# Optimization experiments

Measured on AMD Instinct MI355X. Metric: run time of the kernel, lower is better.

The kernel has to match this reference:

```python
import jax, jax.numpy as jnp
import numpy as np
from math import sqrt

B, L, H, D = 4, 4096, 8, 64
FACTOR = 5


def setup_inputs():
    key = jax.random.key(0)
    k1, k2, k3, k4 = jax.random.split(key, 4)
    queries = jax.random.normal(k1, (B, L, H, D), dtype=jnp.float32)
    keys = jax.random.normal(k2, (B, L, H, D), dtype=jnp.float32)
    values = jax.random.normal(k3, (B, L, H, D), dtype=jnp.float32)
    sample_k = min(FACTOR * int(np.ceil(np.log(L))), L)  # U_part = 45
    index_sample = jax.random.randint(k4, (L, sample_k), 0, L)
    return {"queries": queries, "keys": keys, "values": values,
            "index_sample": index_sample}


def reference(queries, keys, values, index_sample):
    Bq, L_Q, Hq, Dq = queries.shape
    L_K = keys.shape[1]
    Q = jnp.transpose(queries, (0, 2, 1, 3))  # [B,H,L_Q,D]
    K = jnp.transpose(keys, (0, 2, 1, 3))     # [B,H,L_K,D]
    V = jnp.transpose(values, (0, 2, 1, 3))   # [B,H,L_K,D]
    n_top = min(FACTOR * int(np.ceil(np.log(L_Q))), L_Q)  # u = 45

    # --- _prob_QK: randomly-sampled QK scoring + top-k query selection ---
    K_sample = K[:, :, index_sample, :]                       # [B,H,L_Q,sample_k,D]
    Q_K_sample = jnp.einsum('bhld,bhlkd->bhlk', Q, K_sample)  # [B,H,L_Q,sample_k]
    M = Q_K_sample.max(-1) - Q_K_sample.sum(-1) / L_K         # sparsity measure
    _, M_top = jax.lax.top_k(M, n_top)                        # [B,H,u] query indices
    Q_reduce = jnp.take_along_axis(Q, M_top[..., None], axis=2)  # [B,H,u,D]
    scores = jnp.einsum('bhud,bhkd->bhuk', Q_reduce, K)       # [B,H,u,L_K]

    # scale = 1/sqrt(D) (self.scale is None)
    scores = scores * (1.0 / sqrt(Dq))

    # --- ProbMask (mask_flag=True): causal, key j masked if j > query idx ---
    mask = jnp.arange(L_K)[None, None, None, :] > M_top[..., None]
    scores = jnp.where(mask, -jnp.inf, scores)
    attn = jax.nn.softmax(scores, axis=-1)                    # [B,H,u,L_K]

    # --- initial context (masked case): cumulative sum of V over time ---
    context = jnp.cumsum(V, axis=2)                           # [B,H,L_Q,D]

    # --- scatter attn@V into the selected query positions ---
    upd = jnp.einsum('bhuk,bhkd->bhud', attn, V)              # [B,H,u,D]
    b_idx = jnp.arange(Bq)[:, None, None]
    h_idx = jnp.arange(Hq)[None, :, None]
    context = context.at[b_idx, h_idx, M_top].set(upd)
    return context  # [B,H,L_Q,D], as returned by the torch module
```

## Files before the change

### kernel.cpp

```cpp
#include <hip/hip_runtime.h>

#define NB 4
#define LSEQ 4096
#define NH 8
#define ND 64
#define NSAMP 45
#define NTOP 45

typedef float f32x4 __attribute__((ext_vector_type(4)));

__global__ __launch_bounds__(256) void prep_kernel(
        const int* __restrict__ idxS, int* __restrict__ sortedPack) {
    int t = threadIdx.x;
    int l = blockIdx.x * 256 + t;
    const int* is = idxS + (size_t)l * NSAMP;
    __shared__ int cnt[256][17];
    #pragma unroll
    for (int c = 0; c < 16; ++c) cnt[t][c] = 0;
    for (int s = 0; s < NSAMP; ++s) cnt[t][is[s] >> 8] += 1;
    int run = 0;
    #pragma unroll
    for (int c = 0; c < 16; ++c) { int v = cnt[t][c]; cnt[t][c] = run; run += v; }
    for (int s = 0; s < NSAMP; ++s) {
        int idx = is[s];
        int pos = cnt[t][idx >> 8]++;
        sortedPack[(size_t)l * NSAMP + pos] = (idx << 8) | s;
    }
}

__global__ __launch_bounds__(256, 1) void compute_M_kernel(
        const float* __restrict__ Q,
        const float* __restrict__ K,
        const int* __restrict__ sortedPack,
        float* __restrict__ Mout) {
    int xcd = blockIdx.x & 7;
    int sub = blockIdx.x >> 3;
    int bh  = (xcd << 2) | (sub & 3);
    int lt  = sub >> 2;
    int b = bh >> 3, h = bh & 7;
    int t = threadIdx.x;
    int l0 = (lt << 9) + t;
    int l1 = l0 + 256;

    __shared__ float Ks[256 * 68];
    __shared__ float Plds[512 * 45];

    f32x4 qa[16], qb[16];
    {
        const f32x4* qp0 = reinterpret_cast<const f32x4*>(
            Q + (((size_t)b * LSEQ + l0) * NH + h) * ND);
        const f32x4* qp1 = reinterpret_cast<const f32x4*>(
            Q + (((size_t)b * LSEQ + l1) * NH + h) * ND);
        #pragma unroll
        for (int i = 0; i < 16; ++i) qa[i] = __builtin_nontemporal_load(qp0 + i);
        #pragma unroll
        for (int i = 0; i < 16; ++i) qb[i] = __builtin_nontemporal_load(qp1 + i);
    }

    auto dotQK = [&](const f32x4 (&q4)[16], const float* kr) -> float {
        const f32x4* k4 = reinterpret_cast<const f32x4*>(kr);
        float w[32];
        #pragma unroll
        for (int i = 0; i < 8; ++i) {
            f32x4 a = q4[i], bb = k4[i], c = q4[i + 8], d4 = k4[i + 8];
            w[4 * i + 0] = __fadd_rn(__fmul_rn(a.x, bb.x), __fmul_rn(c.x, d4.x));
            w[4 * i + 1] = __fadd_rn(__fmul_rn(a.y, bb.y), __fmul_rn(c.y, d4.y));
            w[4 * i + 2] = __fadd_rn(__fmul_rn(a.z, bb.z), __fmul_rn(c.z, d4.z));
            w[4 * i + 3] = __fadd_rn(__fmul_rn(a.w, bb.w), __fmul_rn(c.w, d4.w));
        }
        #pragma unroll
        for (int off = 16; off; off >>= 1) {
            #pragma unroll
            for (int i = 0; i < off; ++i) w[i] = __fadd_rn(w[i], w[i + off]);
        }
        return w[0];
    };

    const int* sp0 = sortedPack + (size_t)l0 * NSAMP;
    const int* sp1 = sortedPack + (size_t)l1 * NSAMP;
    int ptr0 = 0, ptr1 = 0;
    int pk0 = sp0[0], pk1 = sp1[0];

    size_t kbh = ((size_t)b * LSEQ * NH + h) * ND;

    for (int c = 0; c < 16; ++c) {
        #pragma unroll
        for (int i = 0; i < 16; ++i) {
            int flat = i * 256 + t;
            int row = flat >> 4, col = flat & 15;
            f32x4 v = *reinterpret_cast<const f32x4*>(
                K + kbh + (size_t)(c * 256 + row) * (NH * ND) + col * 4);
            *reinterpret_cast<f32x4*>(&Ks[row * 68 + col * 4]) = v;
        }
        __syncthreads();

        while ((pk0 >> 16) == c) {
            int r = (pk0 >> 8) & 255;
            int s = pk0 & 255;
            Plds[t * 45 + s] = dotQK(qa, &Ks[r * 68]);
            ++ptr0;
            pk0 = (ptr0 < NSAMP) ? sp0[ptr0] : 0x7fffffff;
        }
        while ((pk1 >> 16) == c) {
            int r = (pk1 >> 8) & 255;
            int s = pk1 & 255;
            Plds[(256 + t) * 45 + s] = dotQK(qb, &Ks[r * 68]);
            ++ptr1;
            pk1 = (ptr1 < NSAMP) ? sp1[ptr1] : 0x7fffffff;
        }
        __syncthreads();
    }

    {
        float maxv = -INFINITY, sumv = 0.0f;
        for (int s = 0; s < NSAMP; ++s) {
            float v = Plds[t * 45 + s];
            maxv = fmaxf(maxv, v);
            sumv = __fadd_rn(sumv, v);
        }
        Mout[(size_t)bh * LSEQ + l0] = maxv - sumv * (1.0f / (float)LSEQ);
    }
    {
        float maxv = -INFINITY, sumv = 0.0f;
        for (int s = 0; s < NSAMP; ++s) {
            float v = Plds[(256 + t) * 45 + s];
            maxv = fmaxf(maxv, v);
            sumv = __fadd_rn(sumv, v);
        }
        Mout[(size_t)bh * LSEQ + l1] = maxv - sumv * (1.0f / (float)LSEQ);
    }
}

__global__ __launch_bounds__(256) void topk_kernel(
        const float* __restrict__ M, int* __restrict__ Mtop) {
    int bh = blockIdx.x;
    int t = threadIdx.x;
    int wave = t >> 6, lane = t & 63;
    const float* m = M + (size_t)bh * LSEQ;

    float rv[16];
    #pragma unroll
    for (int k = 0; k < 16; ++k) rv[k] = m[t + (k << 8)];

    __shared__ float wv[4];
    __shared__ int   wi[4];
    __shared__ int   winIdx;

    for (int iter = 0; iter < NTOP; ++iter) {
        float bv = -INFINITY; int bi = 0x7fffffff;
        #pragma unroll
        for (int k = 0; k < 16; ++k) {
            float v = rv[k];
            if (v > bv) { bv = v; bi = t + (k << 8); }
        }
        #pragma unroll
        for (int off = 1; off < 64; off <<= 1) {
            float ov = __shfl_xor(bv, off, 64);
            int   oi = __shfl_xor(bi, off, 64);
            if (ov > bv || (ov == bv && oi < bi)) { bv = ov; bi = oi; }
        }
        if (lane == 0) { wv[wave] = bv; wi[wave] = bi; }
        __syncthreads();
        if (t == 0) {
            float cv = wv[0]; int ci = wi[0];
            for (int ww = 1; ww < 4; ++ww) {
                if (wv[ww] > cv || (wv[ww] == cv && wi[ww] < ci)) { cv = wv[ww]; ci = wi[ww]; }
            }
            winIdx = ci;
            Mtop[bh * NTOP + iter] = ci;
        }
        __syncthreads();
        int widx = winIdx;
        #pragma unroll
        for (int k = 0; k < 16; ++k)
            if (widx == t + (k << 8)) rv[k] = -INFINITY;
        __syncthreads();
    }
}

__global__ __launch_bounds__(256) void cumsumA_kernel(
        const float* __restrict__ V, float* __restrict__ chunkSums) {
    int blk = blockIdx.x;
    int c = blk & 15;
    int bh = blk >> 4;
    int h = bh & (NH - 1);
    int b = bh >> 3;
    int g = threadIdx.x >> 6, d = threadIdx.x & 63;

    const size_t rstride = (size_t)NH * ND;
    size_t vbase = (size_t)b * LSEQ * rstride + (size_t)h * ND + d;

    int l0 = c * 256 + g * 64;
    float s = 0.0f;
    for (int l = l0; l < l0 + 64; ++l) s += V[vbase + (size_t)l * rstride];

    __shared__ float part[4][ND];
    part[g][d] = s;
    __syncthreads();
    if (threadIdx.x < ND)
        chunkSums[(size_t)blk * ND + d] =
            part[0][d] + part[1][d] + part[2][d] + part[3][d];
}

__global__ __launch_bounds__(256) void cumsumC_kernel(
        const float* __restrict__ V, const float* __restrict__ chunkSums,
        float* __restrict__ out) {
    int blk = blockIdx.x;
    int c = blk & 15;
    int bh = blk >> 4;
    int h = bh & (NH - 1);
    int b = bh >> 3;
    int g = threadIdx.x >> 6, d = threadIdx.x & 63;

    const size_t rstride = (size_t)NH * ND;
    size_t vbase = (size_t)b * LSEQ * rstride + (size_t)h * ND + d;

    float run = 0.0f;
    for (int cc = 0; cc < c; ++cc)
        run += chunkSums[((size_t)bh * 16 + cc) * ND + d];

    int l0 = c * 256 + g * 64;
    float s = 0.0f;
    for (int l = l0; l < l0 + 64; ++l) s += V[vbase + (size_t)l * rstride];
    __shared__ float part[4][ND];
    part[g][d] = s;
    __syncthreads();
    for (int gg = 0; gg < g; ++gg) run += part[gg][d];

    size_t obase = (size_t)bh * LSEQ * ND + d;
    for (int l = l0; l < l0 + 64; ++l) {
        run += V[vbase + (size_t)l * rstride];
        out[obase + (size_t)l * ND] = run;
    }
}

#define TJ 64
__global__ __launch_bounds__(256) void attn_rows_kernel(
        const float* __restrict__ Q,
        const float* __restrict__ K,
        const float* __restrict__ V,
        const int* __restrict__ Mtop,
        float* __restrict__ out) {
    int x = blockIdx.x;
    int xcd = x & 7;
    int slot = x >> 3;
    int grp = slot / NTOP;
    int u = slot % NTOP;
    int bh = grp * 8 + xcd;
    int h = bh & (NH - 1);
    int b = bh >> 3;
    int pos = Mtop[bh * NTOP + u];
    int n = pos + 1;
    int t = threadIdx.x;
    int r = t >> 2, qt = t & 3;

    __shared__ float Ks[TJ][65];
    __shared__ float Vs[TJ][65];
    __shared__ float red[256];

    const size_t rstride = (size_t)NH * ND;
    size_t base = (size_t)b * LSEQ * rstride + (size_t)h * ND;

    float qreg[16];
    const float* qrow = Q + base + (size_t)pos * rstride + qt * 16;
    #pragma unroll
    for (int i = 0; i < 16; i += 4) {
        float4 v4 = *reinterpret_cast<const float4*>(qrow + i);
        qreg[i] = v4.x; qreg[i + 1] = v4.y; qreg[i + 2] = v4.z; qreg[i + 3] = v4.w;
    }

    float m = -INFINITY, s = 0.0f;
    float o[16];
    #pragma unroll
    for (int dd = 0; dd < 16; ++dd) o[dd] = 0.0f;

    int ntiles = (n + TJ - 1) / TJ;
    for (int tt = 0; tt < ntiles; ++tt) {
        int j0 = tt * TJ;
        __syncthreads();
        #pragma unroll
        for (int i = 0; i < 4; ++i) {
            int u16 = t + i * 256;
            int rr = u16 >> 4, cc = u16 & 15;
            int j = j0 + rr;
            int jc = (j < n) ? j : (n - 1);
            const float* rowk = K + base + (size_t)jc * rstride;
            float4 kv = *reinterpret_cast<const float4*>(rowk + cc * 4);
            Ks[rr][cc * 4 + 0] = kv.x; Ks[rr][cc * 4 + 1] = kv.y;
            Ks[rr][cc * 4 + 2] = kv.z; Ks[rr][cc * 4 + 3] = kv.w;
            const float* rowv = V + base + (size_t)jc * rstride;
            float4 vv = *reinterpret_cast<const float4*>(rowv + cc * 4);
            Vs[rr][cc * 4 + 0] = vv.x; Vs[rr][cc * 4 + 1] = vv.y;
            Vs[rr][cc * 4 + 2] = vv.z; Vs[rr][cc * 4 + 3] = vv.w;
        }
        __syncthreads();

        int j = j0 + r;
        float acc = 0.0f;
        #pragma unroll
        for (int dd = 0; dd < 16; ++dd)
            acc = fmaf(qreg[dd], Ks[r][qt * 16 + dd], acc);
        acc += __shfl_xor(acc, 1, 64);
        acc += __shfl_xor(acc, 2, 64);

        if (j < n) {
            float sc = acc * 0.125f;
            if (sc > m) {
                float alpha = __expf(m - sc);
                s *= alpha;
                #pragma unroll
                for (int dd = 0; dd < 16; ++dd) o[dd] *= alpha;
                m = sc;
            }
            float e = __expf(sc - m);
            s += e;
            #pragma unroll
            for (int dd = 0; dd < 16; ++dd)
                o[dd] = fmaf(e, Vs[r][qt * 16 + dd], o[dd]);
        }
    }
    __syncthreads();

    red[t] = m; __syncthreads();
    for (int sft = 128; sft; sft >>= 1) {
        if (t < sft) red[t] = fmaxf(red[t], red[t + sft]);
        __syncthreads();
    }
    float mstar = red[0]; __syncthreads();
    float a = __expf(m - mstar);

    red[t] = s * a; __syncthreads();
    for (int sft = 128; sft; sft >>= 1) {
        if (t < sft) red[t] += red[t + sft];
        __syncthreads();
    }
    float S = red[0]; __syncthreads();

    float* OB = &Ks[0][0];
    #pragma unroll
    for (int dd = 0; dd < 16; ++dd) OB[t * 16 + dd] = o[dd] * a;
    __syncthreads();

    if (t < ND) {
        int qtt = t >> 4, dd = t & 15;
        float tot = 0.0f;
        for (int k = 0; k < 64; ++k) tot += OB[(4 * k + qtt) * 16 + dd];
        out[((size_t)bh * LSEQ + pos) * ND + t] = tot / S;
    }
}

extern "C" void kernel_launch(void* const* d_in, const int* in_sizes, int n_in,
                              void* d_out, int out_size, void* d_ws, size_t ws_size,
                              hipStream_t stream) {
    const float* Q = (const float*)d_in[0];
    const float* K = (const float*)d_in[1];
    const float* V = (const float*)d_in[2];
    const int* idxS = (const int*)d_in[3];
    float* out = (float*)d_out;

    float* Mbuf = (float*)d_out;
    int*   sortedPack = (int*)((char*)d_out + (1 << 20));
    int*   Mtop = (int*)d_ws;
    float* chunkSums = (float*)((char*)d_ws + 8192);

    prep_kernel<<<LSEQ / 256, 256, 0, stream>>>(idxS, sortedPack);
    compute_M_kernel<<<256, 256, 0, stream>>>(Q, K, sortedPack, Mbuf);
    topk_kernel<<<NB * NH, 256, 0, stream>>>(Mbuf, Mtop);
    cumsumA_kernel<<<NB * NH * 16, 256, 0, stream>>>(V, chunkSums);
    cumsumC_kernel<<<NB * NH * 16, 256, 0, stream>>>(V, chunkSums, out);
    attn_rows_kernel<<<NB * NH * NTOP, 256, 0, stream>>>(Q, K, V, Mtop, out);
}
```

Before: 500.2 us.

## Split attention over key chunks with shared K/V tiles and merge partials

Replaces the per-query-row attention kernel with a flash-style split: each block handles one (batch, head) and a 256-key chunk for all 45 selected queries. K and V tiles are loaded once per chunk and reused across queries, with an online softmax. Partial max, sum and output are written to scratch in the output buffer, merged by a second kernel, and scattered after the cumsum so the scratch is overwritten. This adds two small kernels and scratch traffic, and keeps a fallback path when the workspace is too small.

```diff
diff --git a/kernel.cpp b/kernel.cpp
--- a/kernel.cpp
+++ b/kernel.cpp
@@ -6,6 +6,8 @@
 #define ND 64
 #define NSAMP 45
 #define NTOP 45
+#define ACH 256
+#define NCH (LSEQ / ACH)
 
 typedef float f32x4 __attribute__((ext_vector_type(4)));
 
@@ -232,6 +234,156 @@
         run += V[vbase + (size_t)l * rstride];
         out[obase + (size_t)l * ND] = run;
     }
+}
+
+__global__ __launch_bounds__(256, 1) void attn_partial_kernel(
+        const float* __restrict__ Q, const float* __restrict__ K,
+        const float* __restrict__ V, const int* __restrict__ Mtop,
+        float* __restrict__ part) {
+    int bh = blockIdx.x >> 4;
+    int c  = blockIdx.x & 15;
+    int b = bh >> 3, h = bh & 7;
+    int t = threadIdx.x;
+    int w = t >> 6, lane = t & 63;
+    int jj = lane >> 4, dq = lane & 15;
+
+    __shared__ float Qs[NTOP * ND];
+    __shared__ int   posS[NTOP];
+    __shared__ float Vs[64][68];
+    __shared__ float Pw[4][64];
+
+    size_t base = ((size_t)b * LSEQ * NH + h) * ND;
+
+    if (t < NTOP) posS[t] = Mtop[bh * NTOP + t];
+    __syncthreads();
+    for (int idx = t; idx < NTOP * 16; idx += 256) {
+        int u = idx >> 4, cg = idx & 15;
+        f32x4 v = *reinterpret_cast<const f32x4*>(
+            Q + base + (size_t)posS[u] * (NH * ND) + cg * 4);
+        *reinterpret_cast<f32x4*>(&Qs[u * ND + cg * 4]) = v;
+    }
+
+    f32x4 o[12];
+    float mreg[12], sreg[12];
+    #pragma unroll
+    for (int qi = 0; qi < 12; ++qi) {
+        o[qi] = 0.0f; mreg[qi] = -INFINITY; sreg[qi] = 0.0f;
+    }
+
+    for (int tt = 0; tt < ACH / 64; ++tt) {
+        int tile0 = c * ACH + tt * 64;
+        __syncthreads();
+        #pragma unroll
+        for (int i = 0; i < 4; ++i) {
+            int flat = i * 256 + t;
+            int r = flat >> 4, cg = flat & 15;
+            f32x4 v = *reinterpret_cast<const f32x4*>(
+                V + base + (size_t)(tile0 + r) * (NH * ND) + cg * 4);
+            *reinterpret_cast<f32x4*>(&Vs[r][cg * 4]) = v;
+        }
+        __syncthreads();
+
+        f32x4 kreg[16];
+        #pragma unroll
+        for (int i = 0; i < 16; ++i)
+            kreg[i] = *reinterpret_cast<const f32x4*>(
+                K + base + (size_t)(tile0 + lane) * (NH * ND) + i * 4);
+
+        #pragma unroll
+        for (int qi = 0; qi < 12; ++qi) {
+            int u = w + 4 * qi;
+            if (u >= NTOP) continue;
+            int pu = posS[u];
+            if (pu < tile0) continue;
+
+            float a0 = 0, a1 = 0, a2 = 0, a3 = 0;
+            #pragma unroll
+            for (int di = 0; di < 16; ++di) {
+                f32x4 qv = *reinterpret_cast<const f32x4*>(&Qs[u * ND + di * 4]);
+                a0 = fmaf(qv.x, kreg[di].x, a0);
+                a1 = fmaf(qv.y, kreg[di].y, a1);
+                a2 = fmaf(qv.z, kreg[di].z, a2);
+                a3 = fmaf(qv.w, kreg[di].w, a3);
+            }
+            float sc = ((a0 + a1) + (a2 + a3)) * 0.125f;
+            if (tile0 + lane > pu) sc = -INFINITY;
+
+            float tmax = sc;
+            #pragma unroll
+            for (int off = 1; off < 64; off <<= 1)
+                tmax = fmaxf(tmax, __shfl_xor(tmax, off, 64));
+            float mold = mreg[qi];
+            float mnew = fmaxf(mold, tmax);
+            float alpha = __expf(mold - mnew);
+            float e = __expf(sc - mnew);
+            float esum = e;
+            #pragma unroll
+            for (int off = 1; off < 64; off <<= 1)
+                esum += __shfl_xor(esum, off, 64);
+            sreg[qi] = sreg[qi] * alpha + esum;
+            mreg[qi] = mnew;
+            Pw[w][lane] = e;
+            o[qi] *= alpha;
+            #pragma unroll
+            for (int i = 0; i < 16; ++i) {
+                float pe = Pw[w][i * 4 + jj];
+                f32x4 vv = *reinterpret_cast<const f32x4*>(&Vs[i * 4 + jj][dq * 4]);
+                o[qi] += vv * pe;
+            }
+        }
+    }
+
+    #pragma unroll
+    for (int qi = 0; qi < 12; ++qi) {
+        int u = w + 4 * qi;
+        if (u >= NTOP) continue;
+        if (posS[u] < c * ACH) continue;
+        f32x4 oo = o[qi];
+        #pragma unroll
+        for (int off = 16; off <= 32; off <<= 1) {
+            oo.x += __shfl_xor(oo.x, off, 64);
+            oo.y += __shfl_xor(oo.y, off, 64);
+            oo.z += __shfl_xor(oo.z, off, 64);
+            oo.w += __shfl_xor(oo.w, off, 64);
+        }
+        size_t pb = ((size_t)(bh * NTOP + u) * NCH + c) * 72;
+        if (lane < 16)
+            *reinterpret_cast<f32x4*>(&part[pb + 4 + dq * 4]) = oo;
+        if (lane == 0) { part[pb] = mreg[qi]; part[pb + 1] = sreg[qi]; }
+    }
+}
+
+__global__ __launch_bounds__(256) void attn_merge_kernel(
+        const float* __restrict__ part, const int* __restrict__ Mtop,
+        float* __restrict__ ctx) {
+    int j = blockIdx.x * 4 + (threadIdx.x >> 6);
+    int lane = threadIdx.x & 63;
+    int bh = j / NTOP, u = j - bh * NTOP;
+    int pos = Mtop[bh * NTOP + u];
+    int cmax = pos >> 8;
+    size_t pb0 = (size_t)(bh * NTOP + u) * NCH * 72;
+    float m = -INFINITY;
+    for (int cc = 0; cc <= cmax; ++cc)
+        m = fmaxf(m, part[pb0 + (size_t)cc * 72]);
+    float S = 0.0f, oacc = 0.0f;
+    for (int cc = 0; cc <= cmax; ++cc) {
+        float mc = part[pb0 + (size_t)cc * 72];
+        float sc = part[pb0 + (size_t)cc * 72 + 1];
+        float wgt = __expf(mc - m);
+        S = fmaf(sc, wgt, S);
+        oacc = fmaf(part[pb0 + (size_t)cc * 72 + 4 + lane], wgt, oacc);
+    }
+    ctx[(size_t)j * ND + lane] = oacc / S;
+}
+
+__global__ __launch_bounds__(256) void scatter_kernel(
+        const float* __restrict__ ctx, const int* __restrict__ Mtop,
+        float* __restrict__ out) {
+    int j = blockIdx.x * 4 + (threadIdx.x >> 6);
+    int lane = threadIdx.x & 63;
+    int bh = j / NTOP, u = j - bh * NTOP;
+    int pos = Mtop[bh * NTOP + u];
+    out[((size_t)bh * LSEQ + pos) * ND + lane] = ctx[(size_t)j * ND + lane];
 }
 
 #define TJ 64
@@ -360,13 +512,25 @@
 
     float* Mbuf = (float*)d_out;
     int*   sortedPack = (int*)((char*)d_out + (1 << 20));
+    float* part = (float*)((char*)d_out + (2 << 20));
     int*   Mtop = (int*)d_ws;
     float* chunkSums = (float*)((char*)d_ws + 8192);
+    float* ctx = (float*)((char*)d_ws + 8192 + 131072);
+    size_t wsNeeded = 8192 + 131072 + (size_t)NB * NH * NTOP * ND * 4;
 
     prep_kernel<<<LSEQ / 256, 256, 0, stream>>>(idxS, sortedPack);
     compute_M_kernel<<<256, 256, 0, stream>>>(Q, K, sortedPack, Mbuf);
     topk_kernel<<<NB * NH, 256, 0, stream>>>(Mbuf, Mtop);
-    cumsumA_kernel<<<NB * NH * 16, 256, 0, stream>>>(V, chunkSums);
-    cumsumC_kernel<<<NB * NH * 16, 256, 0, stream>>>(V, chunkSums, out);
-    attn_rows_kernel<<<NB * NH * NTOP, 256, 0, stream>>>(Q, K, V, Mtop, out);
-}
+
+    if (ws_size >= wsNeeded) {
+        attn_partial_kernel<<<NB * NH * NCH, 256, 0, stream>>>(Q, K, V, Mtop, part);
+        attn_merge_kernel<<<NB * NH * NTOP / 4, 256, 0, stream>>>(part, Mtop, ctx);
+        cumsumA_kernel<<<NB * NH * 16, 256, 0, stream>>>(V, chunkSums);
+        cumsumC_kernel<<<NB * NH * 16, 256, 0, stream>>>(V, chunkSums, out);
+        scatter_kernel<<<NB * NH * NTOP / 4, 256, 0, stream>>>(ctx, Mtop, out);
+    } else {
+        cumsumA_kernel<<<NB * NH * 16, 256, 0, stream>>>(V, chunkSums);
+        cumsumC_kernel<<<NB * NH * 16, 256, 0, stream>>>(V, chunkSums, out);
+        attn_rows_kernel<<<NB * NH * NTOP, 256, 0, stream>>>(Q, K, V, Mtop, out);
+    }
+}
```

Result: faster. 436.6 us (-12.7%).
